# Kernel tuning notes

Measured on AMD Instinct MI355X. Metric: run time of the kernel, lower is better.

## Reference

```python
import jax, jax.numpy as jnp
import numpy as np

B, DIM, H, W = 16, 512, 32, 32
CH = DIM // 2        # per-branch channels
RED = CH // 4        # reduction channels in kernel generator
EPS_BN, EPS_FN, EPS_LN = 1e-5, 1e-6, 1e-6


def _conv1d(x, w):
    # x: (B, Cin, L), w: (Cout, Cin, 3), 'same' padding
    return jax.lax.conv_general_dilated(x, w, (1,), [(1, 1)],
                                        dimension_numbers=('NCH', 'OIH', 'NCH'))


def _gen(g, g1w, bng, bnb, bnrm, bnrv, g2w, fns, fnm):
    # kernel generator (gen_type='CONV', act=Hardswish) + FilterNorm
    # g: (B, CH, L) -> (B, CH, L)
    h = _conv1d(g, g1w)
    h = (h - bnrm[None, :, None]) * jax.lax.rsqrt(bnrv[None, :, None] + EPS_BN) \
        * bng[None, :, None] + bnb[None, :, None]          # eval-mode BatchNorm
    h = jax.nn.hard_swish(h)
    h = _conv1d(h, g2w)
    u = jnp.mean(h, axis=(1, 2), keepdims=True)            # FilterNorm: per-sample
    s = jnp.mean((h - u) ** 2, axis=(1, 2), keepdims=True)
    return (h - u) * jax.lax.rsqrt(s + EPS_FN) * fns[None] + fnm[None]


def _branch(x, pe, g1w, bng, bnb, bnrm, bnrv, g2w, fns, fnm, bias, axis):
    # dygcc_Conv2d: axis==2 -> type 'H' (full-length circular kernel along H),
    # axis==3 -> type 'W'. The torch cat-trick grouped conv2d with groups=B*C is
    # exactly a per-(b,c) circular cross-correlation; we express it as a batched
    # circulant matmul.
    x = x + (pe[None, :, :, None] if axis == 2 else pe[None, :, None, :])
    glob = jnp.mean(x, axis=(2, 3))                        # (B,C) global avg pool
    info = jnp.mean(x, axis=5 - axis)                      # (B,C,L) mean over other axis
    w = _gen(info + glob[:, :, None], g1w, bng, bnb, bnrm, bnrv, g2w, fns, fnm)  # (B,C,L)
    L = w.shape[-1]
    idx = (jnp.arange(L)[None, :] - jnp.arange(L)[:, None]) % L
    M = w[:, :, idx]                                       # M[b,c,i,j] = w[b,c,(j-i)%L]
    if axis == 2:
        out = jnp.einsum('bcij,bcjw->bciw', M, x)
    else:
        out = jnp.einsum('bcij,bchj->bchi', M, x)
    return out + bias[None, :, None, None]


def _forward(x, pe_h, g1w_h, bng_h, bnb_h, bnrm_h, bnrv_h, g2w_h, fns_h, fnm_h, bias_h,
             pe_w, g1w_w, bng_w, bnb_w, bnrm_w, bnrv_w, g2w_w, fns_w, fnm_w, bias_w,
             ln_w, ln_b, pw1_w, pw1_b, pw2_w, pw2_b, gamma):
    inp = x
    x1, x2 = x[:, :CH], x[:, CH:]
    y1 = _branch(x1, pe_h, g1w_h, bng_h, bnb_h, bnrm_h, bnrv_h, g2w_h, fns_h, fnm_h, bias_h, 2)
    y2 = _branch(x2, pe_w, g1w_w, bng_w, bnb_w, bnrm_w, bnrv_w, g2w_w, fns_w, fnm_w, bias_w, 3)
    y = jnp.concatenate([y1, y2], axis=1).transpose(0, 2, 3, 1)   # (B,H,W,DIM)
    mu = jnp.mean(y, axis=-1, keepdims=True)
    var = jnp.mean((y - mu) ** 2, axis=-1, keepdims=True)
    y = (y - mu) * jax.lax.rsqrt(var + EPS_LN) * ln_w + ln_b      # LayerNorm channels_last
    y = jax.nn.gelu(y @ pw1_w + pw1_b, approximate=False) @ pw2_w + pw2_b
    y = gamma * y
    return inp + y.transpose(0, 3, 1, 2)


def setup_inputs() -> dict:
    key = jax.random.key(0)
    ks = jax.random.split(key, 32)
    def n(i, shape, s=1.0):
        return jax.random.normal(ks[i], shape, dtype=jnp.float32) * s
    def branch_params(i0, L):
        return {
            'pe': n(i0, (CH, L), 0.02),
            'g1w': n(i0 + 1, (RED, CH, 3), 0.1),
            'bng': jnp.ones((RED,), jnp.float32),
            'bnb': jnp.zeros((RED,), jnp.float32),
            'bnrm': n(i0 + 2, (RED,), 0.1),
            'bnrv': jax.random.uniform(ks[i0 + 3], (RED,), jnp.float32, 0.5, 1.5),
            'g2w': n(i0 + 4, (CH, RED, 3), 0.1),
            'fns': n(i0 + 5, (CH, L)),
            'fnm': n(i0 + 6, (CH, L)),
            'bias': n(i0 + 7, (CH,), 0.02),
        }
    ph = branch_params(1, H)
    pw = branch_params(10, W)
    return {
        'x': n(0, (B, DIM, H, W)),
        'pe_h': ph['pe'], 'g1w_h': ph['g1w'], 'bng_h': ph['bng'], 'bnb_h': ph['bnb'],
        'bnrm_h': ph['bnrm'], 'bnrv_h': ph['bnrv'], 'g2w_h': ph['g2w'],
        'fns_h': ph['fns'], 'fnm_h': ph['fnm'], 'bias_h': ph['bias'],
        'pe_w': pw['pe'], 'g1w_w': pw['g1w'], 'bng_w': pw['bng'], 'bnb_w': pw['bnb'],
        'bnrm_w': pw['bnrm'], 'bnrv_w': pw['bnrv'], 'g2w_w': pw['g2w'],
        'fns_w': pw['fns'], 'fnm_w': pw['fnm'], 'bias_w': pw['bias'],
        'ln_w': jnp.ones((DIM,), jnp.float32), 'ln_b': jnp.zeros((DIM,), jnp.float32),
        'pw1_w': n(20, (DIM, 4 * DIM), 0.02), 'pw1_b': jnp.zeros((4 * DIM,), jnp.float32),
        'pw2_w': n(21, (4 * DIM, DIM), 0.02), 'pw2_b': jnp.zeros((DIM,), jnp.float32),
        'gamma': jnp.full((DIM,), 1e-6, jnp.float32),
    }


def reference(x, pe_h, g1w_h, bng_h, bnb_h, bnrm_h, bnrv_h, g2w_h, fns_h, fnm_h, bias_h,
              pe_w, g1w_w, bng_w, bnb_w, bnrm_w, bnrv_w, g2w_w, fns_w, fnm_w, bias_w,
              ln_w, ln_b, pw1_w, pw1_b, pw2_w, pw2_b, gamma):
    return _forward(x, pe_h, g1w_h, bng_h, bnb_h, bnrm_h, bnrv_h, g2w_h, fns_h, fnm_h, bias_h,
                    pe_w, g1w_w, bng_w, bnb_w, bnrm_w, bnrv_w, g2w_w, fns_w, fnm_w, bias_w,
                    ln_w, ln_b, pw1_w, pw1_b, pw2_w, pw2_b, gamma)
```

## Files before the change

### kernel.cpp

```cpp
#include <hip/hip_runtime.h>
#include <stdint.h>

#define BB    16
#define DIMC  512
#define CHC   256
#define REDC  64
#define LL    32
#define NTOK  (BB*LL*LL)

typedef unsigned short u16;
typedef unsigned char  u8;
typedef __attribute__((ext_vector_type(4))) float f32x4;

__device__ __forceinline__ float bf2f(u16 u){
  union { unsigned int i; float f; } v; v.i = ((unsigned int)u) << 16; return v.f;
}
__device__ __forceinline__ u16 f2bf(float f){
  union { float f; unsigned int i; } v; v.f = f;
  unsigned int r = (v.i + 0x7FFFu + ((v.i >> 16) & 1u)) >> 16;
  return (u16)r;
}
__device__ __forceinline__ unsigned int pk4_fp8(float a, float b, float c, float d){
  unsigned int w = 0;
  w = __builtin_amdgcn_cvt_pk_fp8_f32(a, b, w, false);
  w = __builtin_amdgcn_cvt_pk_fp8_f32(c, d, w, true);
  return w;
}
__device__ __forceinline__ u8 f2fp8(float f){
  return (u8)(__builtin_amdgcn_cvt_pk_fp8_f32(f, f, 0, false) & 0xffu);
}

__device__ __forceinline__ void gload16(const u8* g, u8* l) {
  __builtin_amdgcn_global_load_lds(
      (const __attribute__((address_space(1))) void*)g,
      (__attribute__((address_space(3))) void*)l, 16, 0, 0);
}

__global__ __launch_bounds__(256) void k_pre(const float* __restrict__ s1,
    u8* __restrict__ d1, const float* __restrict__ s2, u8* __restrict__ d2,
    const float* __restrict__ x, const float* __restrict__ pe_h,
    const float* __restrict__ pe_w, float* __restrict__ g)
{
  int tid = threadIdx.x;
  if (blockIdx.x < 512) {
    __shared__ float tf[64][65];
    int bid = blockIdx.x;
    const float* src; u8* dst; int K, N, n0, k0;
    if (bid < 256) { src = s1; dst = d1; K = 512;  N = 2048; n0 = (bid & 31) * 64; k0 = (bid >> 5) * 64; }
    else { bid -= 256; src = s2; dst = d2; K = 2048; N = 512; n0 = (bid & 7) * 64; k0 = (bid >> 3) * 64; }
    #pragma unroll
    for (int i = 0; i < 16; ++i) {
      int idx = i*256 + tid; int r = idx >> 6, c = idx & 63;
      tf[r][c] = src[(size_t)(k0 + r) * N + n0 + c];
    }
    __syncthreads();
    int c = tid >> 2, gq = tid & 3;
    uint4 o;
    unsigned int* op = (unsigned int*)&o;
    #pragma unroll
    for (int d = 0; d < 4; ++d) {
      int j = gq*16 + d*4;
      op[d] = pk4_fp8(tf[j+0][c], tf[j+1][c], tf[j+2][c], tf[j+3][c]);
    }
    *(uint4*)(dst + (size_t)(n0 + c)*K + k0 + gq*16) = o;
    return;
  }
  int bc = blockIdx.x - 512;
  int br = (bc & 511) >> 8, c = bc & 255;
  __shared__ float tt[32][33];
  const float* xp = x + (size_t)bc * 1024;
  float4 v = ((const float4*)xp)[tid];
  int h = tid >> 3, w4 = (tid & 7) * 4;
  tt[h][w4+0] = v.x; tt[h][w4+1] = v.y; tt[h][w4+2] = v.z; tt[h][w4+3] = v.w;
  __syncthreads();
  if (tid < 32) {
    float rs = 0.f;
    if (br == 0) {
      #pragma unroll
      for (int w = 0; w < 32; ++w) rs += tt[tid][w];
    } else {
      #pragma unroll
      for (int h2 = 0; h2 < 32; ++h2) rs += tt[h2][tid];
    }
    float tot = rs;
    #pragma unroll
    for (int off = 16; off >= 1; off >>= 1) tot += __shfl_xor(tot, off);
    const float* pe = (br == 0 ? pe_h : pe_w) + c*32;
    float pv = pe[tid];
    float pm = pv;
    #pragma unroll
    for (int off = 16; off >= 1; off >>= 1) pm += __shfl_xor(pm, off);
    int b = bc >> 9;
    float gv = rs * (1.f/32.f) + tot * (1.f/1024.f) + pv + pm * (1.f/32.f);
    g[((size_t)(br*BB + b)*256 + c)*32 + tid] = gv;
  }
}

__global__ __launch_bounds__(256) void k_gen1(const float* __restrict__ g,
    float* __restrict__ part, const float* __restrict__ g1w_h,
    const float* __restrict__ g1w_w)
{
  int blk = blockIdx.x; int g32 = blk >> 2, cq = blk & 3;
  int br = g32 >> 4;
  const float* g1w = br ? g1w_w : g1w_h;
  __shared__ float gs[64][34];
  int tid = threadIdx.x;
  const float* gb = g + (size_t)g32 * 8192 + cq*64*32;
  if (tid < 64) { gs[tid][0] = 0.f; gs[tid][33] = 0.f; }
  #pragma unroll
  for (int it = 0; it < 8; ++it) {
    int idx = it*256 + tid;
    gs[idx >> 5][1 + (idx & 31)] = gb[idx];
  }
  __syncthreads();
  int r = tid >> 2, l0 = (tid & 3) * 8;
  float acc[8];
  #pragma unroll
  for (int j = 0; j < 8; ++j) acc[j] = 0.f;
  for (int c = 0; c < 64; ++c) {
    const float* wp = g1w + (r*256 + cq*64 + c)*3;
    float w0 = wp[0], w1 = wp[1], w2 = wp[2];
    float gv[10];
    #pragma unroll
    for (int q = 0; q < 10; ++q) gv[q] = gs[c][l0 + q];
    #pragma unroll
    for (int j = 0; j < 8; ++j) acc[j] += w0*gv[j] + w1*gv[j+1] + w2*gv[j+2];
  }
  float* po = part + (size_t)blk*2048 + r*32 + l0;
  #pragma unroll
  for (int j = 0; j < 8; ++j) po[j] = acc[j];
}

__global__ __launch_bounds__(256) void k_gen2(const float* __restrict__ part,
    float* __restrict__ wout,
    const float* bng_h, const float* bnb_h, const float* bnrm_h, const float* bnrv_h,
    const float* g2w_h, const float* fns_h, const float* fnm_h,
    const float* bng_w, const float* bnb_w, const float* bnrm_w, const float* bnrv_w,
    const float* g2w_w, const float* fns_w, const float* fnm_w)
{
  int g32 = blockIdx.x; int br = g32 >> 4;
  const float* bng  = br ? bng_w  : bng_h;
  const float* bnb  = br ? bnb_w  : bnb_h;
  const float* bnrm = br ? bnrm_w : bnrm_h;
  const float* bnrv = br ? bnrv_w : bnrv_h;
  const float* g2w  = br ? g2w_w  : g2w_h;
  const float* fns  = br ? fns_w  : fns_h;
  const float* fnm  = br ? fnm_w  : fnm_h;

  __shared__ float h1[64][34];
  __shared__ float red[8];
  int tid = threadIdx.x;
  if (tid < 64) { h1[tid][0] = 0.f; h1[tid][33] = 0.f; }
  {
    int r = tid >> 2, l0 = (tid & 3) * 8;
    const float* p0 = part + (size_t)(g32*4 + 0)*2048 + r*32 + l0;
    const float* p1 = part + (size_t)(g32*4 + 1)*2048 + r*32 + l0;
    const float* p2 = part + (size_t)(g32*4 + 2)*2048 + r*32 + l0;
    const float* p3 = part + (size_t)(g32*4 + 3)*2048 + r*32 + l0;
    float sc = bng[r] * rsqrtf(bnrv[r] + 1e-5f);
    float sh = bnb[r] - bnrm[r] * sc;
    #pragma unroll
    for (int j = 0; j < 8; ++j) {
      float v2 = (p0[j] + p1[j] + p2[j] + p3[j])*sc + sh;
      float hs = v2 * fminf(fmaxf(v2 + 3.f, 0.f), 6.f) * (1.f/6.f);
      h1[r][1 + l0 + j] = hs;
    }
  }
  __syncthreads();

  int c = tid;
  float a2[32];
  #pragma unroll
  for (int l = 0; l < 32; ++l) a2[l] = 0.f;
  for (int r = 0; r < 64; ++r) {
    const float* wp = g2w + (c*64 + r)*3;
    float w0 = wp[0], w1 = wp[1], w2 = wp[2];
    float hv[34];
    #pragma unroll
    for (int q = 0; q < 34; ++q) hv[q] = h1[r][q];
    #pragma unroll
    for (int l = 0; l < 32; ++l) a2[l] += w0*hv[l] + w1*hv[l+1] + w2*hv[l+2];
  }
  float s = 0.f, sq = 0.f;
  #pragma unroll
  for (int l = 0; l < 32; ++l) { s += a2[l]; sq += a2[l]*a2[l]; }
  #pragma unroll
  for (int off = 32; off >= 1; off >>= 1) { s += __shfl_xor(s, off); sq += __shfl_xor(sq, off); }
  int wid = tid >> 6;
  if ((tid & 63) == 0) { red[wid*2] = s; red[wid*2+1] = sq; }
  __syncthreads();
  float S  = red[0] + red[2] + red[4] + red[6];
  float SQ = red[1] + red[3] + red[5] + red[7];
  float u   = S * (1.f/8192.f);
  float var = SQ * (1.f/8192.f) - u*u;
  float inv = rsqrtf(var + 1e-6f);
  float* wo = wout + (size_t)g32*8192 + c*32;
  #pragma unroll
  for (int l = 0; l < 32; ++l)
    wo[l] = (a2[l] - u)*inv*fns[c*32 + l] + fnm[c*32 + l];
}

__global__ __launch_bounds__(256) void k_circ(const float* __restrict__ x,
    const float* __restrict__ pe_h, const float* __restrict__ pe_w,
    const float* __restrict__ bias_h, const float* __restrict__ bias_w,
    const float* __restrict__ wgt, u16* __restrict__ ybr)
{
  int bc = blockIdx.x;
  int b = bc >> 9, ch = bc & 511, br = ch >> 8, c = ch & 255;
  __shared__ float xs[32][36];
  __shared__ float ww[32];
  int tid = threadIdx.x;
  const float* xp = x + (size_t)bc * 1024;
  float4 v = ((const float4*)xp)[tid];
  int h = tid >> 3, w4 = (tid & 7) * 4;
  if (br == 0) {
    float p = pe_h[c*32 + h];
    float4 sv; sv.x = v.x + p; sv.y = v.y + p; sv.z = v.z + p; sv.w = v.w + p;
    *(float4*)&xs[h][w4] = sv;
  } else {
    float4 pw = *(const float4*)(pe_w + c*32 + w4);
    float4 sv; sv.x = v.x + pw.x; sv.y = v.y + pw.y; sv.z = v.z + pw.z; sv.w = v.w + pw.w;
    *(float4*)&xs[h][w4] = sv;
  }
  if (tid < 32) ww[tid] = wgt[((size_t)(br*BB + b)*256 + c)*32 + tid];
  __syncthreads();
  float bias = (br ? bias_w : bias_h)[c];
  int i = tid >> 3;
  float o0 = bias, o1 = bias, o2 = bias, o3 = bias;
  if (br == 0) {
    #pragma unroll
    for (int k = 0; k < 32; ++k) {
      float wk = ww[k]; int rr = (i + k) & 31;
      float4 xv = *(const float4*)&xs[rr][w4];
      o0 += wk*xv.x; o1 += wk*xv.y; o2 += wk*xv.z; o3 += wk*xv.w;
    }
  } else {
    #pragma unroll
    for (int k = 0; k < 32; ++k) {
      float wk = ww[k];
      o0 += wk*xs[i][(w4+0+k) & 31]; o1 += wk*xs[i][(w4+1+k) & 31];
      o2 += wk*xs[i][(w4+2+k) & 31]; o3 += wk*xs[i][(w4+3+k) & 31];
    }
  }
  ushort4 o; o.x = f2bf(o0); o.y = f2bf(o1); o.z = f2bf(o2); o.w = f2bf(o3);
  ((ushort4*)(ybr + (size_t)bc * 1024))[tid] = o;
}

__global__ __launch_bounds__(256) void k_ln(const u16* __restrict__ ybr,
    const float* __restrict__ ln_w, const float* __restrict__ ln_b,
    u8* __restrict__ A8)
{
  int bh = blockIdx.x; int b = bh >> 5, h = bh & 31;
  __shared__ float ys[512][33];
  __shared__ float ps[8][32], pq[8][32];
  __shared__ float mus[32], rstds[32];
  __shared__ float lw[512], lb[512];
  int tid = threadIdx.x;
  lw[tid]       = ln_w[tid];       lb[tid]       = ln_b[tid];
  lw[tid + 256] = ln_w[tid + 256]; lb[tid + 256] = ln_b[tid + 256];
  #pragma unroll
  for (int it = 0; it < 16; ++it) {
    int vid = it*256 + tid; int ch = vid >> 3; int w4 = (vid & 7) * 4;
    ushort4 v = *(const ushort4*)(ybr + (size_t)(b*512 + ch)*1024 + h*32 + w4);
    ys[ch][w4+0] = bf2f(v.x); ys[ch][w4+1] = bf2f(v.y);
    ys[ch][w4+2] = bf2f(v.z); ys[ch][w4+3] = bf2f(v.w);
  }
  __syncthreads();
  int w = tid & 31, gq = tid >> 5;
  float s = 0.f, sq = 0.f;
  for (int cc = gq*64; cc < gq*64 + 64; ++cc) { float vv = ys[cc][w]; s += vv; sq += vv*vv; }
  ps[gq][w] = s; pq[gq][w] = sq;
  __syncthreads();
  if (tid < 32) {
    float S = 0.f, SQ = 0.f;
    #pragma unroll
    for (int q = 0; q < 8; ++q) { S += ps[q][tid]; SQ += pq[q][tid]; }
    float mu = S * (1.f/512.f);
    float var = SQ * (1.f/512.f) - mu*mu;
    mus[tid] = mu; rstds[tid] = rsqrtf(var + 1e-6f);
  }
  __syncthreads();
  u8* Arow = A8 + (size_t)(b*1024 + h*32) * 512;
  #pragma unroll
  for (int it = 0; it < 16; ++it) {
    int idx = it*256 + tid;
    int w2 = idx >> 7, cg = idx & 127; int cc = cg*4;
    float mu = mus[w2], rs2 = rstds[w2];
    float v0 = (ys[cc+0][w2] - mu) * rs2 * lw[cc+0] + lb[cc+0];
    float v1 = (ys[cc+1][w2] - mu) * rs2 * lw[cc+1] + lb[cc+1];
    float v2 = (ys[cc+2][w2] - mu) * rs2 * lw[cc+2] + lb[cc+2];
    float v3 = (ys[cc+3][w2] - mu) * rs2 * lw[cc+3] + lb[cc+3];
    ((unsigned int*)(Arow + (size_t)w2*512))[cg] = pk4_fp8(v0, v1, v2, v3);
  }
}

template<int EPI>
__global__ __launch_bounds__(512, 6) void k_gemm(
    const u8* __restrict__ A, const u8* __restrict__ BT,
    void* __restrict__ outv, const float* __restrict__ xin,
    const float* __restrict__ bias, const float* __restrict__ gamma,
    int K, int N, int a_row_off, int out_row_off)
{
  __shared__ u8 As[3][8192];
  __shared__ u8 Bs[3][8192];
  int tid = threadIdx.x;
  int m0 = blockIdx.x * 128, n0 = blockIdx.y * 128;
  int lane = tid & 63, wid = tid >> 6;
  int wr = wid >> 1, wc = wid & 1;
  f32x4 acc[2][4];
  #pragma unroll
  for (int mi = 0; mi < 2; ++mi)
    #pragma unroll
    for (int ni = 0; ni < 4; ++ni) acc[mi][ni] = (f32x4){0.f,0.f,0.f,0.f};

  int rloc = (wid << 4) + (lane >> 2);
  int swzr = ((rloc >> 1) ^ (rloc >> 3)) & 3;
  int cp   = (lane & 3) ^ swzr;
  const u8* aSrc = A  + (size_t)(a_row_off + m0 + rloc)*K + cp*16;
  const u8* bSrc = BT + (size_t)(n0 + rloc)*K + cp*16;
  int ldsOff = wid * 1024;

  auto stage = [&](int t, int slot) {
    int k0 = t << 6;
    gload16(aSrc + k0, &As[slot][ldsOff]);
    gload16(bSrc + k0, &Bs[slot][ldsOff]);
  };
  auto lds8 = [&](const u8* base, int row, int kk, int q) -> long {
    int j = (kk >> 4) + (q >> 1);
    int sz = ((row >> 1) ^ (row >> 3)) & 3;
    int byte = row*64 + ((j ^ sz) << 4) + ((q & 1) << 3);
    return *(const long*)(base + byte);
  };

  int nt = K >> 6;
  stage(0, 0);
  stage(1, 1);

  int sr = 0;
  for (int t = 0; t < nt; ++t) {
    if (t + 2 < nt) {
      int sw = (sr == 0) ? 2 : sr - 1;
      stage(t + 2, sw);
      asm volatile("s_waitcnt vmcnt(4)" ::: "memory");
    } else if (t + 1 < nt) {
      asm volatile("s_waitcnt vmcnt(2)" ::: "memory");
    } else {
      asm volatile("s_waitcnt vmcnt(0)" ::: "memory");
    }
    __builtin_amdgcn_s_barrier();
    const u8* Ar = &As[sr][0];
    const u8* Br = &Bs[sr][0];
    int q = lane >> 4;
    #pragma unroll
    for (int kk = 0; kk < 64; kk += 32) {
      long af[2], bfr[4];
      #pragma unroll
      for (int mi = 0; mi < 2; ++mi)
        af[mi] = lds8(Ar, wr*32 + mi*16 + (lane & 15), kk, q);
      #pragma unroll
      for (int ni = 0; ni < 4; ++ni)
        bfr[ni] = lds8(Br, wc*64 + ni*16 + (lane & 15), kk, q);
      #pragma unroll
      for (int mi = 0; mi < 2; ++mi)
        #pragma unroll
        for (int ni = 0; ni < 4; ++ni)
          acc[mi][ni] = __builtin_amdgcn_mfma_f32_16x16x32_fp8_fp8(af[mi], bfr[ni], acc[mi][ni], 0, 0, 0);
    }
    __builtin_amdgcn_s_barrier();
    sr = (sr == 2) ? 0 : sr + 1;
  }

  if (EPI == 1) {
    __builtin_amdgcn_s_barrier();
    u8* eb = &As[0][0] + wid * 2560;
    #pragma unroll
    for (int mi = 0; mi < 2; ++mi) {
      #pragma unroll
      for (int ni = 0; ni < 4; ++ni) {
        int n = n0 + wc*64 + ni*16 + (lane & 15);
        float bn = bias[n];
        int col = ni*16 + (lane & 15);
        #pragma unroll
        for (int r = 0; r < 4; ++r) {
          int lrow = mi*16 + (lane >> 4)*4 + r;
          float v = acc[mi][ni][r] + bn;
          float hs = fminf(fmaxf(0.2837f * v + 0.5f, 0.f), 1.f);
          eb[lrow*80 + col] = f2fp8(v * hs);
        }
      }
    }
    asm volatile("s_waitcnt lgkmcnt(0)" ::: "memory");
    int lr = lane >> 1, h2 = lane & 1;
    uint4 w0 = *(const uint4*)(eb + lr*80 + h2*32);
    uint4 w1 = *(const uint4*)(eb + lr*80 + h2*32 + 16);
    u8* zrow = (u8*)outv + (size_t)(m0 + wr*32 + lr)*N + n0 + wc*64 + h2*32;
    *(uint4*)(zrow)      = w0;
    *(uint4*)(zrow + 16) = w1;
  } else {
    #pragma unroll
    for (int mi = 0; mi < 2; ++mi) {
      #pragma unroll
      for (int ni = 0; ni < 4; ++ni) {
        int n = n0 + wc*64 + ni*16 + (lane & 15);
        float bn = bias[n];
        float gm = gamma[n];
        int mb = m0 + wr*32 + mi*16 + (lane >> 4)*4;
        int mg = out_row_off + mb;
        int bb = mg >> 10, hh = (mg >> 5) & 31, wv = mg & 31;
        size_t oi = ((size_t)(bb*512 + n))*1024 + hh*32 + wv;
        float4 xv = *(const float4*)(xin + oi);
        float4 ov;
        ov.x = xv.x + gm * (acc[mi][ni][0] + bn);
        ov.y = xv.y + gm * (acc[mi][ni][1] + bn);
        ov.z = xv.z + gm * (acc[mi][ni][2] + bn);
        ov.w = xv.w + gm * (acc[mi][ni][3] + bn);
        *(float4*)((float*)outv + oi) = ov;
      }
    }
  }
}

extern "C" void kernel_launch(void* const* d_in, const int* in_sizes, int n_in,
                              void* d_out, int out_size, void* d_ws, size_t ws_size,
                              hipStream_t stream)
{
  const float* x      = (const float*)d_in[0];
  const float* pe_h   = (const float*)d_in[1];
  const float* g1w_h  = (const float*)d_in[2];
  const float* bng_h  = (const float*)d_in[3];
  const float* bnb_h  = (const float*)d_in[4];
  const float* bnrm_h = (const float*)d_in[5];
  const float* bnrv_h = (const float*)d_in[6];
  const float* g2w_h  = (const float*)d_in[7];
  const float* fns_h  = (const float*)d_in[8];
  const float* fnm_h  = (const float*)d_in[9];
  const float* bias_h = (const float*)d_in[10];
  const float* pe_w   = (const float*)d_in[11];
  const float* g1w_w  = (const float*)d_in[12];
  const float* bng_w  = (const float*)d_in[13];
  const float* bnb_w  = (const float*)d_in[14];
  const float* bnrm_w = (const float*)d_in[15];
  const float* bnrv_w = (const float*)d_in[16];
  const float* g2w_w  = (const float*)d_in[17];
  const float* fns_w  = (const float*)d_in[18];
  const float* fnm_w  = (const float*)d_in[19];
  const float* bias_w = (const float*)d_in[20];
  const float* ln_w   = (const float*)d_in[21];
  const float* ln_b   = (const float*)d_in[22];
  const float* pw1w   = (const float*)d_in[23];
  const float* pw1b   = (const float*)d_in[24];
  const float* pw2w   = (const float*)d_in[25];
  const float* pw2b   = (const float*)d_in[26];
  const float* gamma  = (const float*)d_in[27];
  float* out = (float*)d_out;

  char* ws = (char*)d_ws;
  size_t off = 0;
  auto carve = [&](size_t bytes) -> void* {
    void* p = ws + off; off += (bytes + 255) & ~(size_t)255; return p;
  };
  float* g    = (float*)carve((size_t)2*BB*256*32*4);
  float* wgt  = (float*)carve((size_t)2*BB*256*32*4);
  float* part = (float*)carve((size_t)128*2048*4);
  u8* BT1     = (u8*)carve((size_t)2048*512);
  u8* BT2     = (u8*)carve((size_t)512*2048);
  u8* Abuf    = (u8*)carve((size_t)NTOK*512);
  size_t tail = off;
  u16* ybr = (u16*)(ws + tail);
  u8*  Z   = (u8*)(ws + tail);
  size_t ybr_bytes = (size_t)NTOK*512*2;
  int nch = 1;
  while (nch < 16) {
    size_t zb = ((size_t)NTOK/nch)*2048;
    size_t need = tail + (zb > ybr_bytes ? zb : ybr_bytes);
    if (need <= ws_size) break;
    nch *= 2;
  }

  k_pre<<<512 + BB*512, 256, 0, stream>>>(pw1w, BT1, pw2w, BT2, x, pe_h, pe_w, g);
  k_gen1<<<128, 256, 0, stream>>>(g, part, g1w_h, g1w_w);
  k_gen2<<<32, 256, 0, stream>>>(part, wgt,
      bng_h, bnb_h, bnrm_h, bnrv_h, g2w_h, fns_h, fnm_h,
      bng_w, bnb_w, bnrm_w, bnrv_w, g2w_w, fns_w, fnm_w);
  k_circ<<<BB*512, 256, 0, stream>>>(x, pe_h, pe_w, bias_h, bias_w, wgt, ybr);
  k_ln<<<BB*LL, 256, 0, stream>>>(ybr, ln_w, ln_b, Abuf);

  int Mc = NTOK / nch;
  for (int ci = 0; ci < nch; ++ci) {
    int moff = ci * Mc;
    k_gemm<1><<<dim3(Mc/128, 2048/128), 512, 0, stream>>>(
        Abuf, BT1, Z, nullptr, pw1b, nullptr, 512, 2048, moff, 0);
    k_gemm<2><<<dim3(Mc/128, 512/128), 512, 0, stream>>>(
        Z, BT2, out, x, pw2b, gamma, 2048, 512, 0, moff);
  }
}
```

Baseline: 167.1 us.

## Split kernel-generator second conv across 128 blocks with separate FilterNorm kernel

The second generator conv (k_gen2) now runs on 128 blocks instead of 32. Each block computes a quarter of the output channels, with its weights staged in shared memory and 8 outputs per thread instead of 32. Per-block partial sums and sums of squares are written to global memory, and a new k_gen3 kernel combines them to apply FilterNorm with float4 loads and stores. The aim is to fix the low occupancy and register-heavy serial loop of the old 32-block kernel on a many-CU GPU. The cost is one extra kernel launch and a round trip of the intermediate results through global memory.

```diff
diff --git a/kernel.cpp b/kernel.cpp
--- a/kernel.cpp
+++ b/kernel.cpp
@@ -132,27 +132,27 @@
 }
 
 __global__ __launch_bounds__(256) void k_gen2(const float* __restrict__ part,
-    float* __restrict__ wout,
+    float* __restrict__ a2buf, float* __restrict__ sred,
     const float* bng_h, const float* bnb_h, const float* bnrm_h, const float* bnrv_h,
-    const float* g2w_h, const float* fns_h, const float* fnm_h,
-    const float* bng_w, const float* bnb_w, const float* bnrm_w, const float* bnrv_w,
-    const float* g2w_w, const float* fns_w, const float* fnm_w)
-{
-  int g32 = blockIdx.x; int br = g32 >> 4;
+    const float* g2w_h, const float* bng_w, const float* bnb_w,
+    const float* bnrm_w, const float* bnrv_w, const float* g2w_w)
+{
+  int blk = blockIdx.x; int g32 = blk >> 2, cq = blk & 3;
+  int br = g32 >> 4;
   const float* bng  = br ? bng_w  : bng_h;
   const float* bnb  = br ? bnb_w  : bnb_h;
   const float* bnrm = br ? bnrm_w : bnrm_h;
   const float* bnrv = br ? bnrv_w : bnrv_h;
   const float* g2w  = br ? g2w_w  : g2w_h;
-  const float* fns  = br ? fns_w  : fns_h;
-  const float* fnm  = br ? fnm_w  : fnm_h;
 
   __shared__ float h1[64][34];
+  __shared__ float wlds[64*195];
   __shared__ float red[8];
   int tid = threadIdx.x;
-  if (tid < 64) { h1[tid][0] = 0.f; h1[tid][33] = 0.f; }
+
   {
     int r = tid >> 2, l0 = (tid & 3) * 8;
+    if ((tid & 3) == 0) { h1[r][0] = 0.f; h1[r][33] = 0.f; }
     const float* p0 = part + (size_t)(g32*4 + 0)*2048 + r*32 + l0;
     const float* p1 = part + (size_t)(g32*4 + 1)*2048 + r*32 + l0;
     const float* p2 = part + (size_t)(g32*4 + 2)*2048 + r*32 + l0;
@@ -166,38 +166,75 @@
       h1[r][1 + l0 + j] = hs;
     }
   }
-  __syncthreads();
-
-  int c = tid;
-  float a2[32];
-  #pragma unroll
-  for (int l = 0; l < 32; ++l) a2[l] = 0.f;
+  {
+    const float* wsrc = g2w + cq*12288;
+    #pragma unroll
+    for (int it = 0; it < 48; ++it) {
+      int i = it*256 + tid;
+      int cl = i / 192;
+      int rem = i - cl*192;
+      wlds[cl*195 + rem] = wsrc[i];
+    }
+  }
+  __syncthreads();
+
+  int cl = tid >> 2, l0 = (tid & 3) * 8;
+  const float* wp = &wlds[cl*195];
+  float a2[8];
+  #pragma unroll
+  for (int j = 0; j < 8; ++j) a2[j] = 0.f;
   for (int r = 0; r < 64; ++r) {
-    const float* wp = g2w + (c*64 + r)*3;
-    float w0 = wp[0], w1 = wp[1], w2 = wp[2];
-    float hv[34];
-    #pragma unroll
-    for (int q = 0; q < 34; ++q) hv[q] = h1[r][q];
-    #pragma unroll
-    for (int l = 0; l < 32; ++l) a2[l] += w0*hv[l] + w1*hv[l+1] + w2*hv[l+2];
+    float w0 = wp[r*3+0], w1 = wp[r*3+1], w2 = wp[r*3+2];
+    float hv[10];
+    #pragma unroll
+    for (int q = 0; q < 10; ++q) hv[q] = h1[r][l0 + q];
+    #pragma unroll
+    for (int j = 0; j < 8; ++j) a2[j] += w0*hv[j] + w1*hv[j+1] + w2*hv[j+2];
   }
   float s = 0.f, sq = 0.f;
   #pragma unroll
-  for (int l = 0; l < 32; ++l) { s += a2[l]; sq += a2[l]*a2[l]; }
+  for (int j = 0; j < 8; ++j) { s += a2[j]; sq += a2[j]*a2[j]; }
   #pragma unroll
   for (int off = 32; off >= 1; off >>= 1) { s += __shfl_xor(s, off); sq += __shfl_xor(sq, off); }
-  int wid = tid >> 6;
-  if ((tid & 63) == 0) { red[wid*2] = s; red[wid*2+1] = sq; }
-  __syncthreads();
-  float S  = red[0] + red[2] + red[4] + red[6];
-  float SQ = red[1] + red[3] + red[5] + red[7];
+  if ((tid & 63) == 0) { red[(tid >> 6)*2] = s; red[(tid >> 6)*2+1] = sq; }
+  __syncthreads();
+  if (tid == 0) {
+    sred[blk*2+0] = red[0] + red[2] + red[4] + red[6];
+    sred[blk*2+1] = red[1] + red[3] + red[5] + red[7];
+  }
+  float* ao = a2buf + (size_t)(g32*256 + cq*64 + cl)*32 + l0;
+  #pragma unroll
+  for (int j = 0; j < 8; ++j) ao[j] = a2[j];
+}
+
+__global__ __launch_bounds__(256) void k_gen3(const float* __restrict__ a2buf,
+    const float* __restrict__ sred, float* __restrict__ wout,
+    const float* fns_h, const float* fnm_h,
+    const float* fns_w, const float* fnm_w)
+{
+  int g32 = blockIdx.x; int br = g32 >> 4;
+  const float* fns = br ? fns_w : fns_h;
+  const float* fnm = br ? fnm_w : fnm_h;
+  float S  = sred[g32*8+0] + sred[g32*8+2] + sred[g32*8+4] + sred[g32*8+6];
+  float SQ = sred[g32*8+1] + sred[g32*8+3] + sred[g32*8+5] + sred[g32*8+7];
   float u   = S * (1.f/8192.f);
   float var = SQ * (1.f/8192.f) - u*u;
   float inv = rsqrtf(var + 1e-6f);
+  int c = threadIdx.x;
+  const float* ai = a2buf + (size_t)(g32*256 + c)*32;
   float* wo = wout + (size_t)g32*8192 + c*32;
   #pragma unroll
-  for (int l = 0; l < 32; ++l)
-    wo[l] = (a2[l] - u)*inv*fns[c*32 + l] + fnm[c*32 + l];
+  for (int v4 = 0; v4 < 8; ++v4) {
+    float4 av = *(const float4*)(ai + v4*4);
+    float4 fs = *(const float4*)(fns + c*32 + v4*4);
+    float4 fm = *(const float4*)(fnm + c*32 + v4*4);
+    float4 ov;
+    ov.x = (av.x - u)*inv*fs.x + fm.x;
+    ov.y = (av.y - u)*inv*fs.y + fm.y;
+    ov.z = (av.z - u)*inv*fs.z + fm.z;
+    ov.w = (av.w - u)*inv*fs.w + fm.w;
+    *(float4*)(wo + v4*4) = ov;
+  }
 }
 
 __global__ __launch_bounds__(256) void k_circ(const float* __restrict__ x,
@@ -462,6 +499,8 @@
   float* g    = (float*)carve((size_t)2*BB*256*32*4);
   float* wgt  = (float*)carve((size_t)2*BB*256*32*4);
   float* part = (float*)carve((size_t)128*2048*4);
+  float* a2b  = (float*)carve((size_t)32*256*32*4);
+  float* sred = (float*)carve((size_t)128*2*4);
   u8* BT1     = (u8*)carve((size_t)2048*512);
   u8* BT2     = (u8*)carve((size_t)512*2048);
   u8* Abuf    = (u8*)carve((size_t)NTOK*512);
@@ -479,9 +518,10 @@
 
   k_pre<<<512 + BB*512, 256, 0, stream>>>(pw1w, BT1, pw2w, BT2, x, pe_h, pe_w, g);
   k_gen1<<<128, 256, 0, stream>>>(g, part, g1w_h, g1w_w);
-  k_gen2<<<32, 256, 0, stream>>>(part, wgt,
-      bng_h, bnb_h, bnrm_h, bnrv_h, g2w_h, fns_h, fnm_h,
-      bng_w, bnb_w, bnrm_w, bnrv_w, g2w_w, fns_w, fnm_w);
+  k_gen2<<<128, 256, 0, stream>>>(part, a2b, sred,
+      bng_h, bnb_h, bnrm_h, bnrv_h, g2w_h,
+      bng_w, bnb_w, bnrm_w, bnrv_w, g2w_w);
+  k_gen3<<<32, 256, 0, stream>>>(a2b, sred, wgt, fns_h, fnm_h, fns_w, fnm_w);
   k_circ<<<BB*512, 256, 0, stream>>>(x, pe_h, pe_w, bias_h, bias_w, wgt, ybr);
   k_ln<<<BB*LL, 256, 0, stream>>>(ybr, ln_w, ln_b, Abuf);
 
```

Result: faster. 141.8 us (-15.1%).
